# Kernel optimization log

Measured on AMD Instinct MI355X. Metric: run time of the kernel, lower is better.

Reference implementation:

```python
import jax, jax.numpy as jnp
import numpy as np

TOKEN_BITS = 10
CODEBOOK_SIZE = 2 ** TOKEN_BITS  # 1024
COMMITMENT_COST = 0.25
ENTROPY_LOSS_WEIGHT = 0.1
ENTROPY_TEMPERATURE = 0.01
ENTROPY_GAMMA = 1.0
EPS = 1e-5


def _make_codebook():
    bits_to_indices = (2 ** jnp.arange(TOKEN_BITS)).astype(jnp.int32)          # [c]
    all_codes = jnp.arange(CODEBOOK_SIZE, dtype=jnp.int32)                      # [n]
    bits = ((all_codes[:, None] & bits_to_indices) != 0).astype(jnp.float32)    # [n, c]
    codebook = bits * 2.0 - 1.0                                                 # [n, c] in {-1,+1}
    return bits_to_indices, codebook


def setup_inputs() -> dict:
    key = jax.random.key(0)
    z = jax.random.normal(key, (16, TOKEN_BITS, 64, 64), dtype=jnp.float32)
    return {"z": z}


def reference(z):
    bits_to_indices, codebook = _make_codebook()

    # b c h w -> b h w c
    zp = jnp.transpose(z, (0, 2, 3, 1)).astype(jnp.float32)

    # sign quantization to {-1, +1}
    sign_mask = zp > 0.0
    z_q = jnp.where(sign_mask, 1.0, -1.0).astype(jnp.float32)

    # pack sign bits into codebook indices
    min_encoding_indices = jnp.sum(sign_mask.astype(jnp.int32) * bits_to_indices, axis=-1)  # [b,h,w]

    # commitment loss (stop-grad on the quantized target)
    commitment_loss = COMMITMENT_COST * jnp.mean((jax.lax.stop_gradient(z_q) - zp) ** 2)

    # entropy loss: logits = -d = 2 * z . codebook^T, softened by temperature
    logits = 2.0 * jnp.einsum('bhwc,nc->bhwn', zp, codebook)  # [b,h,w,n]
    log_probs = jax.nn.log_softmax(logits / ENTROPY_TEMPERATURE, axis=-1)
    probs = jnp.exp(log_probs)
    per_sample_entropy = jnp.mean(-jnp.sum(probs * log_probs, axis=-1))
    avg_probs = jnp.mean(probs, axis=(0, 1, 2))  # [n]
    avg_entropy = ENTROPY_GAMMA * (-jnp.sum(avg_probs * jnp.log(avg_probs + EPS)))
    entropy_loss = ENTROPY_LOSS_WEIGHT * (per_sample_entropy - avg_entropy)

    loss = commitment_loss + entropy_loss

    # straight-through estimator
    z_quantized = zp + jax.lax.stop_gradient(z_q - zp)
    # b h w c -> b c h w
    z_quantized = jnp.transpose(z_quantized, (0, 3, 1, 2))

    return z_quantized, loss, per_sample_entropy, min_encoding_indices
```

## Files before the change

kernel.cpp:

```cpp
#include <hip/hip_runtime.h>

#define NCH    10
#define NCODE  1024
#define NLOC   65536
#define NZ     655360
#define GRID   1024
#define THR    128
#define LPB    64
#define NHIST  8
#define NPART  (GRID * 2)

__device__ __forceinline__ float wave_reduce_sum(float v) {
#pragma unroll
    for (int off = 32; off > 0; off >>= 1)
        v += __shfl_down(v, off, 64);
    return v;
}

__global__ __launch_bounds__(THR) void lfq_main(
    const float* __restrict__ z, float* __restrict__ out,
    float* __restrict__ wsH, float* __restrict__ wsC, float* __restrict__ wsE)
{
    __shared__ float sR[LPB][NCH];
    __shared__ unsigned short sM[LPB][NCH];

    const int tid  = threadIdx.x;
    const int wv   = tid >> 6;
    const int lane = tid & 63;
    const int sub  = lane >> 5;
    const int l32  = lane & 31;
    const int lloc = wv * 32 + l32;
    const int loc  = blockIdx.x * LPB + lloc;
    const int b    = loc >> 12;
    const int base = b * (NCH * 4096) + (loc & 4095);
    const int c0   = sub * 5;
    float* hist = wsH + (blockIdx.x & (NHIST - 1)) * NCODE;

    float zc[5];
#pragma unroll
    for (int i = 0; i < 5; ++i)
        zc[i] = __builtin_nontemporal_load(z + base + (c0 + i) * 4096);

    float commit = 0.f, ent = 0.f, pstar = 1.f;
    int idx = 0, k = 0;
#pragma unroll
    for (int i = 0; i < 5; ++i) {
        float zv = zc[i];
        bool bit = zv > 0.f;
        float s = bit ? 1.f : -1.f;
        __builtin_nontemporal_store(s, out + base + (c0 + i) * 4096);
        if (bit) idx |= (1 << (c0 + i));
        float d = s - zv;
        commit += d * d;
        float a = fabsf(zv) * 400.f;
        if (a < 23.0f) {
            float e = __expf(-a);
            float inv = 1.f / (1.f + e);
            ent += __logf(1.f + e) + a * e * inv;
            pstar *= inv;
            sR[lloc][c0 + k] = e;
            sM[lloc][c0 + k] = (unsigned short)(1u << (c0 + i));
            ++k;
        }
    }

    const int   idx_o = __shfl_xor(idx, 32, 64);
    const float p_o   = __shfl_xor(pstar, 32, 64);
    const int   k_o   = __shfl_xor(k, 32, 64);

    if (sub == 0) {
        const int idxT = idx | idx_o;
        const float pT = pstar * p_o;
        __builtin_nontemporal_store((float)idxT, out + NZ + 2 + loc);

        atomicAdd(&hist[idxT], pT);
        const int k0 = k, kt = k + k_o;
        for (int m = 1; m < (1 << kt); ++m) {
            float w = pT;
            int code = idxT;
            for (int j = 0; j < kt; ++j)
                if (m & (1 << j)) {
                    const int slot = (j < k0) ? j : (5 + j - k0);
                    w *= sR[lloc][slot];
                    code ^= sM[lloc][slot];
                }
            atomicAdd(&hist[code], w);
        }
    }

    float cw = wave_reduce_sum(commit);
    float ew = wave_reduce_sum(ent);
    if (lane == 0) {
        wsC[blockIdx.x * 2 + wv] = cw;
        wsE[blockIdx.x * 2 + wv] = ew;
    }
}

__global__ __launch_bounds__(1024) void lfq_final(
    const float* __restrict__ wsH, const float* __restrict__ wsC,
    const float* __restrict__ wsE, float* __restrict__ out)
{
    const int n = threadIdx.x;
    float s = 0.f;
#pragma unroll
    for (int h = 0; h < NHIST; ++h) s += wsH[h * NCODE + n];
    float avg_p = s * (1.f / (float)NLOC);
    float term = -avg_p * __logf(avg_p + 1e-5f);
    float c = wsC[n] + wsC[1024 + n];
    float e = wsE[n] + wsE[1024 + n];
    float tw = wave_reduce_sum(term);
    float cw = wave_reduce_sum(c);
    float ew = wave_reduce_sum(e);
    __shared__ float red[48];
    const int wave = n >> 6, lane = n & 63;
    if (lane == 0) { red[wave] = tw; red[16 + wave] = cw; red[32 + wave] = ew; }
    __syncthreads();
    if (n == 0) {
        float avg_ent = 0.f, cs = 0.f, es = 0.f;
#pragma unroll
        for (int w = 0; w < 16; ++w) {
            avg_ent += red[w]; cs += red[16 + w]; es += red[32 + w];
        }
        float commitment = 0.25f * cs * (1.f / (float)NZ);
        float per_sample = es * (1.f / (float)NLOC);
        out[NZ]     = commitment + 0.1f * (per_sample - avg_ent);
        out[NZ + 1] = per_sample;
    }
}

extern "C" void kernel_launch(void* const* d_in, const int* in_sizes, int n_in,
                              void* d_out, int out_size, void* d_ws, size_t ws_size,
                              hipStream_t stream) {
    const float* z = (const float*)d_in[0];
    float* out = (float*)d_out;
    float* wsH = (float*)d_ws;
    float* wsC = wsH + NHIST * NCODE;
    float* wsE = wsC + NPART;

    lfq_main<<<GRID, THR, 0, stream>>>(z, out, wsH, wsC, wsE);
    lfq_final<<<1, 1024, 0, stream>>>(wsH, wsC, wsE, out);
}
```

Baseline: 72.02 us.

## Accumulate code histogram in shared memory per block, reduce partials in separate kernel

Each block now builds the soft-probability histogram in LDS with shared atomics instead of global atomics on 8 contended copies, then writes a per-block partial histogram. A new kernel reduces the 256 partial histograms and computes the average-entropy term, and the final kernel sums those block results. Blocks grow to 512 threads covering 256 locations each. This removes contended global atomics but adds a third kernel launch, extra syncs and a 1 MB partial-histogram write and read.

```diff
diff --git a/kernel.cpp b/kernel.cpp
--- a/kernel.cpp
+++ b/kernel.cpp
@@ -4,11 +4,11 @@
 #define NCODE  1024
 #define NLOC   65536
 #define NZ     655360
-#define GRID   1024
-#define THR    128
-#define LPB    64
-#define NHIST  8
-#define NPART  (GRID * 2)
+#define GRID   256
+#define THR    512
+#define LPB    256
+#define NPART  (GRID * 8)
+#define K2_BLK 16
 
 __device__ __forceinline__ float wave_reduce_sum(float v) {
 #pragma unroll
@@ -19,8 +19,9 @@
 
 __global__ __launch_bounds__(THR) void lfq_main(
     const float* __restrict__ z, float* __restrict__ out,
-    float* __restrict__ wsH, float* __restrict__ wsC, float* __restrict__ wsE)
+    float* __restrict__ wsP, float* __restrict__ wsC, float* __restrict__ wsE)
 {
+    __shared__ float hist[NCODE];
     __shared__ float sR[LPB][NCH];
     __shared__ unsigned short sM[LPB][NCH];
 
@@ -34,7 +35,9 @@
     const int b    = loc >> 12;
     const int base = b * (NCH * 4096) + (loc & 4095);
     const int c0   = sub * 5;
-    float* hist = wsH + (blockIdx.x & (NHIST - 1)) * NCODE;
+
+    hist[tid] = 0.f;
+    hist[tid + 512] = 0.f;
 
     float zc[5];
 #pragma unroll
@@ -68,6 +71,8 @@
     const float p_o   = __shfl_xor(pstar, 32, 64);
     const int   k_o   = __shfl_xor(k, 32, 64);
 
+    __syncthreads();
+
     if (sub == 0) {
         const int idxT = idx | idx_o;
         const float pT = pstar * p_o;
@@ -91,35 +96,57 @@
     float cw = wave_reduce_sum(commit);
     float ew = wave_reduce_sum(ent);
     if (lane == 0) {
-        wsC[blockIdx.x * 2 + wv] = cw;
-        wsE[blockIdx.x * 2 + wv] = ew;
+        wsC[blockIdx.x * 8 + wv] = cw;
+        wsE[blockIdx.x * 8 + wv] = ew;
+    }
+
+    __syncthreads();
+    wsP[blockIdx.x * NCODE + tid]       = hist[tid];
+    wsP[blockIdx.x * NCODE + tid + 512] = hist[tid + 512];
+}
+
+__global__ __launch_bounds__(256) void lfq_hist_reduce(
+    const float* __restrict__ wsP, float* __restrict__ wsS)
+{
+    __shared__ float part[4][64];
+    const int t     = threadIdx.x;
+    const int code  = blockIdx.x * 64 + (t & 63);
+    const int chunk = t >> 6;
+    float s = 0.f;
+#pragma unroll 8
+    for (int j = chunk * 64; j < chunk * 64 + 64; ++j)
+        s += wsP[j * NCODE + code];
+    part[chunk][t & 63] = s;
+    __syncthreads();
+    if (t < 64) {
+        float tot = part[0][t] + part[1][t] + part[2][t] + part[3][t];
+        float avg_p = tot * (1.f / (float)NLOC);
+        float term = -avg_p * __logf(avg_p + 1e-5f);
+        float tw = wave_reduce_sum(term);
+        if (t == 0) wsS[blockIdx.x] = tw;
     }
 }
 
 __global__ __launch_bounds__(1024) void lfq_final(
-    const float* __restrict__ wsH, const float* __restrict__ wsC,
-    const float* __restrict__ wsE, float* __restrict__ out)
+    const float* __restrict__ wsC, const float* __restrict__ wsE,
+    const float* __restrict__ wsS, float* __restrict__ out)
 {
     const int n = threadIdx.x;
-    float s = 0.f;
-#pragma unroll
-    for (int h = 0; h < NHIST; ++h) s += wsH[h * NCODE + n];
-    float avg_p = s * (1.f / (float)NLOC);
-    float term = -avg_p * __logf(avg_p + 1e-5f);
     float c = wsC[n] + wsC[1024 + n];
     float e = wsE[n] + wsE[1024 + n];
-    float tw = wave_reduce_sum(term);
+    float s = (n < K2_BLK) ? wsS[n] : 0.f;
     float cw = wave_reduce_sum(c);
     float ew = wave_reduce_sum(e);
+    float sw = wave_reduce_sum(s);
     __shared__ float red[48];
     const int wave = n >> 6, lane = n & 63;
-    if (lane == 0) { red[wave] = tw; red[16 + wave] = cw; red[32 + wave] = ew; }
+    if (lane == 0) { red[wave] = cw; red[16 + wave] = ew; red[32 + wave] = sw; }
     __syncthreads();
     if (n == 0) {
-        float avg_ent = 0.f, cs = 0.f, es = 0.f;
+        float cs = 0.f, es = 0.f, avg_ent = 0.f;
 #pragma unroll
         for (int w = 0; w < 16; ++w) {
-            avg_ent += red[w]; cs += red[16 + w]; es += red[32 + w];
+            cs += red[w]; es += red[16 + w]; avg_ent += red[32 + w];
         }
         float commitment = 0.25f * cs * (1.f / (float)NZ);
         float per_sample = es * (1.f / (float)NLOC);
@@ -133,10 +160,12 @@
                               hipStream_t stream) {
     const float* z = (const float*)d_in[0];
     float* out = (float*)d_out;
-    float* wsH = (float*)d_ws;
-    float* wsC = wsH + NHIST * NCODE;
+    float* wsP = (float*)d_ws;
+    float* wsC = wsP + GRID * NCODE;
     float* wsE = wsC + NPART;
+    float* wsS = wsE + NPART;
 
-    lfq_main<<<GRID, THR, 0, stream>>>(z, out, wsH, wsC, wsE);
-    lfq_final<<<1, 1024, 0, stream>>>(wsH, wsC, wsE, out);
+    lfq_main<<<GRID, THR, 0, stream>>>(z, out, wsP, wsC, wsE);
+    lfq_hist_reduce<<<K2_BLK, 256, 0, stream>>>(wsP, wsS);
+    lfq_final<<<1, 1024, 0, stream>>>(wsC, wsE, wsS, out);
 }
```

Measured after the change: 76.17 us. 1.06x slower.
